# Kernel tuning notes

Measured on AMD Instinct MI355X. Metric: run time of the kernel, lower is better.

The kernel has to match this reference:

```python
import math
import jax, jax.numpy as jnp
import numpy as np

NEG_BIG = -1e12  # matches torch's -1000000000000.0 padding


def setup_inputs() -> dict:
    key = jax.random.key(0)
    k1, k2, k3 = jax.random.split(key, 3)
    bs, n_tok, n_heads, width = 1, 4096, 8, 64
    dst_mxlen, src_mxlen = 32, 64
    q = jax.random.normal(k1, (bs, n_tok, n_heads, width), dtype=jnp.float32)
    k = jax.random.normal(k2, (bs, n_tok, n_heads, width), dtype=jnp.float32)
    v = jax.random.normal(k3, (bs, n_tok, n_heads, width), dtype=jnp.float32)
    # Sliding-window COO: each dst attends to its dst_mxlen preceding tokens (clipped).
    dst = jnp.repeat(jnp.arange(n_tok, dtype=jnp.int32), dst_mxlen)
    cnt = jnp.tile(jnp.arange(dst_mxlen, dtype=jnp.int32), n_tok)
    src = jnp.clip(dst - cnt, 0, n_tok - 1)
    coo = jnp.stack([dst, src, cnt], axis=1)  # [cl, 3]
    return {"v": v, "q": q, "k": k, "coo": coo,
            "dst_mxlen": dst_mxlen, "src_mxlen": src_mxlen, "use_softmax": 1}


def reference(v, q, k, coo, dst_mxlen, src_mxlen, use_softmax):
    bs, n_tok, n_heads, width = q.shape
    cl = coo.shape[0]
    # [b, h, t, w] layout
    qq = jnp.transpose(q, (0, 2, 1, 3))[:, :, coo[:, 0], :]  # [b,h,cl,w]
    kk = jnp.transpose(k, (0, 2, 1, 3))[:, :, coo[:, 1], :]
    vv = jnp.transpose(v, (0, 2, 1, 3))
    scale = -1.0 / math.sqrt(width)
    ww = jnp.sum(jnp.abs(qq - kk), axis=-1) * scale  # [b,h,cl]
    # Padded softmax buffer, last slot is the (optional) softmax denominator pad.
    attn = jnp.full((bs, n_heads, n_tok, dst_mxlen + 1), NEG_BIG, dtype=q.dtype)
    attn = attn.at[:, :, coo[:, 0], coo[:, 2]].set(ww)
    if use_softmax:
        attn = attn.at[:, :, :, -1].set(0.0)
        attn_sm = jax.nn.softmax(attn, axis=-1)
    else:
        attn_sm = jnp.exp(attn)
    attn_sm = attn_sm[:, :, :, :-1]  # [b,h,t,s]
    # Scatter V into the padded buffer: vw[b,h,dst,cnt,:] = vv[b,h,src,:]
    vw = jnp.zeros((bs, n_heads, n_tok, dst_mxlen, width), dtype=q.dtype)
    vw = vw.at[:, :, coo[:, 0], coo[:, 2], :].set(vv[:, :, coo[:, 1], :])
    vo = jnp.einsum('bhds,bhdsw->bdhw', attn_sm, vw)
    return vo
```

## Files before the change

### kernel.cpp

```cpp
#include <hip/hip_runtime.h>
#include <math.h>


constexpr int H = 8;
constexpr int W = 64;
constexpr int TPW = 2;

template <int CTRL>
__device__ __forceinline__ float dpp_add(float x) {
    int xi = __builtin_bit_cast(int, x);
    int yi = __builtin_amdgcn_update_dpp(0, xi, CTRL, 0xf, 0xf, true);
    return x + __builtin_bit_cast(float, yi);
}

__device__ __forceinline__ float reduce16(float a) {
    a = dpp_add<0xB1>(a);
    a = dpp_add<0x4E>(a);
    a = dpp_add<0x141>(a);
    a = dpp_add<0x140>(a);
    return a;
}

__global__ __launch_bounds__(256) void l1attn_sparse_kernel(
    const float* __restrict__ v,
    const float* __restrict__ q,
    const float* __restrict__ k,
    const int*   __restrict__ p_dst_mxlen,
    const int*   __restrict__ p_use_softmax,
    float*       __restrict__ out,
    int n_tok)
{
    const int dst_mxlen = *p_dst_mxlen;
    const int use_sm    = *p_use_softmax;

    int bid = blockIdx.x;
    if ((gridDim.x & 7) == 0) {
        const int chunk = gridDim.x >> 3;
        bid = (bid & 7) * chunk + (bid >> 3);
    }

    const int wid  = bid * (blockDim.x >> 6) + (threadIdx.x >> 6);
    const int lane = threadIdx.x & 63;

    const int pairIdx = wid >> 1;
    const int t0 = pairIdx * TPW;
    if (t0 >= n_tok) return;
    const int h     = (wid & 1) * 4 + (lane >> 4);
    const int dbase = (lane & 15) * 4;

    float4 qv[TPW];
    #pragma unroll
    for (int j = 0; j < TPW; ++j) {
        int t = t0 + j; t = t < n_tok ? t : n_tok - 1;
        qv[j] = *reinterpret_cast<const float4*>(q + (t * H + h) * W + dbase);
    }

    float4 acc[TPW];
    float  sump[TPW];
    #pragma unroll
    for (int j = 0; j < TPW; ++j) { acc[j] = {0.f,0.f,0.f,0.f}; sump[j] = 0.f; }

    int s_lo = t0 - (dst_mxlen - 1); s_lo = s_lo < 0 ? 0 : s_lo;
    const int s_hi = (t0 + TPW - 1) < (n_tok - 1) ? (t0 + TPW - 1) : (n_tok - 1);

    #pragma unroll 4
    for (int s = s_lo; s <= s_hi; ++s) {
        const int base = (s * H + h) * W + dbase;
        const float4 kv = *reinterpret_cast<const float4*>(k + base);
        const float4 vv = *reinterpret_cast<const float4*>(v + base);

        #pragma unroll
        for (int j = 0; j < TPW; ++j) {
            const int t = t0 + j;
            float a = fabsf(qv[j].x - kv.x) + fabsf(qv[j].y - kv.y) +
                      fabsf(qv[j].z - kv.z) + fabsf(qv[j].w - kv.w);
            a = reduce16(a);

            float m;
            if (s == 0) {
                int mm = dst_mxlen - t;
                m = (float)(mm > 0 ? mm : 0);
            } else {
                const int c = t - s;
                m = (c >= 0 && c < dst_mxlen) ? 1.f : 0.f;
            }

            const float p = m * __expf(a * -0.125f);
            sump[j] += p;
            acc[j].x += p * vv.x; acc[j].y += p * vv.y;
            acc[j].z += p * vv.z; acc[j].w += p * vv.w;
        }
    }

    #pragma unroll
    for (int j = 0; j < TPW; ++j) {
        const int t = t0 + j;
        if (t < n_tok) {
            const float scale = use_sm ? 1.0f / (1.0f + sump[j]) : 1.0f;
            float4 o = {acc[j].x * scale, acc[j].y * scale,
                        acc[j].z * scale, acc[j].w * scale};
            *reinterpret_cast<float4*>(out + (t * H + h) * W + dbase) = o;
        }
    }
}

extern "C" void kernel_launch(void* const* d_in, const int* in_sizes, int n_in,
                              void* d_out, int out_size, void* d_ws, size_t ws_size,
                              hipStream_t stream) {
    const float* v   = (const float*)d_in[0];
    const float* q   = (const float*)d_in[1];
    const float* k   = (const float*)d_in[2];
    const int*   p_dst_mxlen = (const int*)d_in[4];
    const int*   p_use_sm    = (const int*)d_in[6];
    float* out = (float*)d_out;

    const int n_tok = in_sizes[1] / (H * W);

    const int pairs  = (n_tok + TPW - 1) / TPW;
    const int waves  = pairs * 2;
    const int blocks = (waves + 3) / 4;
    l1attn_sparse_kernel<<<blocks, 256, 0, stream>>>(
        v, q, k, p_dst_mxlen, p_use_sm, out, n_tok);
}
```

Baseline: 21.99 us.

## Split sliding window across two waves per head-half and combine partials via LDS

Each block now handles one token pair. Its four waves cover two head halves times two halves of the source window. The second window-half wave writes its partial accumulators and sums to shared memory, and after a barrier the first wave adds them and writes the output. This shortens each wave's serial loop and doubles the grid size to hide latency better, at the cost of a block barrier, LDS traffic, and half the waves idling during the epilogue.

```diff
diff --git a/kernel.cpp b/kernel.cpp
--- a/kernel.cpp
+++ b/kernel.cpp
@@ -39,13 +39,15 @@
         bid = (bid & 7) * chunk + (bid >> 3);
     }
 
-    const int wid  = bid * (blockDim.x >> 6) + (threadIdx.x >> 6);
+    const int sub  = threadIdx.x >> 6;
     const int lane = threadIdx.x & 63;
+    const int headhalf = sub >> 1;
+    const int winhalf  = sub & 1;
 
-    const int pairIdx = wid >> 1;
-    const int t0 = pairIdx * TPW;
+    const int t0 = bid * TPW;
     if (t0 >= n_tok) return;
-    const int h     = (wid & 1) * 4 + (lane >> 4);
+
+    const int h     = headhalf * 4 + (lane >> 4);
     const int dbase = (lane & 15) * 4;
 
     float4 qv[TPW];
@@ -62,9 +64,13 @@
 
     int s_lo = t0 - (dst_mxlen - 1); s_lo = s_lo < 0 ? 0 : s_lo;
     const int s_hi = (t0 + TPW - 1) < (n_tok - 1) ? (t0 + TPW - 1) : (n_tok - 1);
+    const int len  = s_hi - s_lo + 1;
+    const int half = (len + 1) >> 1;
+    const int my_lo = winhalf ? s_lo + half : s_lo;
+    const int my_hi = winhalf ? s_hi       : s_lo + half - 1;
 
     #pragma unroll 4
-    for (int s = s_lo; s <= s_hi; ++s) {
+    for (int s = my_lo; s <= my_hi; ++s) {
         const int base = (s * H + h) * W + dbase;
         const float4 kv = *reinterpret_cast<const float4*>(k + base);
         const float4 vv = *reinterpret_cast<const float4*>(v + base);
@@ -92,14 +98,34 @@
         }
     }
 
-    #pragma unroll
-    for (int j = 0; j < TPW; ++j) {
-        const int t = t0 + j;
-        if (t < n_tok) {
-            const float scale = use_sm ? 1.0f / (1.0f + sump[j]) : 1.0f;
-            float4 o = {acc[j].x * scale, acc[j].y * scale,
-                        acc[j].z * scale, acc[j].w * scale};
-            *reinterpret_cast<float4*>(out + (t * H + h) * W + dbase) = o;
+    __shared__ float lds[2][TPW][5][64];
+    if (winhalf == 1) {
+        #pragma unroll
+        for (int j = 0; j < TPW; ++j) {
+            lds[headhalf][j][0][lane] = acc[j].x;
+            lds[headhalf][j][1][lane] = acc[j].y;
+            lds[headhalf][j][2][lane] = acc[j].z;
+            lds[headhalf][j][3][lane] = acc[j].w;
+            lds[headhalf][j][4][lane] = sump[j];
+        }
+    }
+    __syncthreads();
+    if (winhalf == 0) {
+        #pragma unroll
+        for (int j = 0; j < TPW; ++j) {
+            acc[j].x += lds[headhalf][j][0][lane];
+            acc[j].y += lds[headhalf][j][1][lane];
+            acc[j].z += lds[headhalf][j][2][lane];
+            acc[j].w += lds[headhalf][j][3][lane];
+            sump[j]  += lds[headhalf][j][4][lane];
+
+            const int t = t0 + j;
+            if (t < n_tok) {
+                const float scale = use_sm ? 1.0f / (1.0f + sump[j]) : 1.0f;
+                float4 o = {acc[j].x * scale, acc[j].y * scale,
+                            acc[j].z * scale, acc[j].w * scale};
+                *reinterpret_cast<float4*>(out + (t * H + h) * W + dbase) = o;
+            }
         }
     }
 }
@@ -116,9 +142,7 @@
 
     const int n_tok = in_sizes[1] / (H * W);
 
-    const int pairs  = (n_tok + TPW - 1) / TPW;
-    const int waves  = pairs * 2;
-    const int blocks = (waves + 3) / 4;
+    const int blocks = (n_tok + TPW - 1) / TPW;
     l1attn_sparse_kernel<<<blocks, 256, 0, stream>>>(
         v, q, k, p_dst_mxlen, p_use_sm, out, n_tok);
 }
```

After: 20.51 us. 6.7% less time.

## Split window over four waves per token block with LDS reduction, packed math

Applied to the files above, without the earlier changes.

Each 512-thread block now handles four tokens across all heads. The source window is split into four quarters, one per wave, and the partial accumulators and softmax sums are combined through shared memory after a barrier. Sharing K/V across four tokens is meant to cut redundant loads, and the split is meant to shorten each wave's serial loop. The abs-diff and accumulate steps use packed 2-wide float vectors to target packed FP32 instructions. This adds LDS traffic, a block-wide sync, and idle waves during the final reduction.

```diff
diff --git a/kernel.cpp b/kernel.cpp
--- a/kernel.cpp
+++ b/kernel.cpp
@@ -2,9 +2,11 @@
 #include <math.h>
 
 
-constexpr int H = 8;
-constexpr int W = 64;
-constexpr int TPW = 2;
+typedef float v2f __attribute__((ext_vector_type(2)));
+
+constexpr int H   = 8;
+constexpr int W   = 64;
+constexpr int TPB = 4;
 
 template <int CTRL>
 __device__ __forceinline__ float dpp_add(float x) {
@@ -21,7 +23,17 @@
     return a;
 }
 
-__global__ __launch_bounds__(256) void l1attn_sparse_kernel(
+__device__ __forceinline__ float absdiff4(float4 qv, float4 kv) {
+    v2f q01 = {qv.x, qv.y}, q23 = {qv.z, qv.w};
+    v2f k01 = {kv.x, kv.y}, k23 = {kv.z, kv.w};
+    v2f d0 = q01 - k01, d1 = q23 - k23;
+    v2f a0 = __builtin_elementwise_max(d0, -d0);
+    v2f a1 = __builtin_elementwise_max(d1, -d1);
+    v2f ss = a0 + a1;
+    return ss.x + ss.y;
+}
+
+__global__ __launch_bounds__(512) void l1attn_sparse_kernel(
     const float* __restrict__ v,
     const float* __restrict__ q,
     const float* __restrict__ k,
@@ -39,67 +51,95 @@
         bid = (bid & 7) * chunk + (bid >> 3);
     }
 
-    const int wid  = bid * (blockDim.x >> 6) + (threadIdx.x >> 6);
+    const int sub  = threadIdx.x >> 6;
     const int lane = threadIdx.x & 63;
+    const int hh   = sub >> 2;
+    const int wq   = sub & 3;
 
-    const int pairIdx = wid >> 1;
-    const int t0 = pairIdx * TPW;
+    const int t0 = bid * TPB;
     if (t0 >= n_tok) return;
-    const int h     = (wid & 1) * 4 + (lane >> 4);
+
+    const int h     = hh * 4 + (lane >> 4);
     const int dbase = (lane & 15) * 4;
 
-    float4 qv[TPW];
+    float4 qv[TPB];
     #pragma unroll
-    for (int j = 0; j < TPW; ++j) {
+    for (int j = 0; j < TPB; ++j) {
         int t = t0 + j; t = t < n_tok ? t : n_tok - 1;
         qv[j] = *reinterpret_cast<const float4*>(q + (t * H + h) * W + dbase);
     }
 
-    float4 acc[TPW];
-    float  sump[TPW];
+    v2f   acc01[TPB], acc23[TPB];
+    float sump[TPB];
     #pragma unroll
-    for (int j = 0; j < TPW; ++j) { acc[j] = {0.f,0.f,0.f,0.f}; sump[j] = 0.f; }
+    for (int j = 0; j < TPB; ++j) {
+        acc01[j] = (v2f){0.f, 0.f}; acc23[j] = (v2f){0.f, 0.f}; sump[j] = 0.f;
+    }
 
     int s_lo = t0 - (dst_mxlen - 1); s_lo = s_lo < 0 ? 0 : s_lo;
-    const int s_hi = (t0 + TPW - 1) < (n_tok - 1) ? (t0 + TPW - 1) : (n_tok - 1);
+    int s_hi = t0 + TPB - 1; s_hi = s_hi < n_tok - 1 ? s_hi : n_tok - 1;
+    const int len  = s_hi - s_lo + 1;
+    const int qlen = (len + 3) >> 2;
+    const int my_lo = s_lo + wq * qlen;
+    int my_hi = my_lo + qlen - 1; my_hi = my_hi < s_hi ? my_hi : s_hi;
 
-    #pragma unroll 4
-    for (int s = s_lo; s <= s_hi; ++s) {
+    #pragma unroll 2
+    for (int s = my_lo; s <= my_hi; ++s) {
         const int base = (s * H + h) * W + dbase;
         const float4 kv = *reinterpret_cast<const float4*>(k + base);
         const float4 vv = *reinterpret_cast<const float4*>(v + base);
+        v2f v01 = {vv.x, vv.y}, v23 = {vv.z, vv.w};
 
         #pragma unroll
-        for (int j = 0; j < TPW; ++j) {
+        for (int j = 0; j < TPB; ++j) {
             const int t = t0 + j;
-            float a = fabsf(qv[j].x - kv.x) + fabsf(qv[j].y - kv.y) +
-                      fabsf(qv[j].z - kv.z) + fabsf(qv[j].w - kv.w);
-            a = reduce16(a);
+            float a = reduce16(absdiff4(qv[j], kv));
 
             float m;
             if (s == 0) {
                 int mm = dst_mxlen - t;
                 m = (float)(mm > 0 ? mm : 0);
             } else {
-                const int c = t - s;
-                m = (c >= 0 && c < dst_mxlen) ? 1.f : 0.f;
+                m = ((unsigned)(t - s) < (unsigned)dst_mxlen) ? 1.f : 0.f;
             }
 
             const float p = m * __expf(a * -0.125f);
             sump[j] += p;
-            acc[j].x += p * vv.x; acc[j].y += p * vv.y;
-            acc[j].z += p * vv.z; acc[j].w += p * vv.w;
+            acc01[j] += p * v01;
+            acc23[j] += p * v23;
         }
     }
 
-    #pragma unroll
-    for (int j = 0; j < TPW; ++j) {
-        const int t = t0 + j;
-        if (t < n_tok) {
-            const float scale = use_sm ? 1.0f / (1.0f + sump[j]) : 1.0f;
-            float4 o = {acc[j].x * scale, acc[j].y * scale,
-                        acc[j].z * scale, acc[j].w * scale};
-            *reinterpret_cast<float4*>(out + (t * H + h) * W + dbase) = o;
+    __shared__ float lds[3][2][TPB][5][64];
+    if (wq != 0) {
+        #pragma unroll
+        for (int j = 0; j < TPB; ++j) {
+            lds[wq - 1][hh][j][0][lane] = acc01[j].x;
+            lds[wq - 1][hh][j][1][lane] = acc01[j].y;
+            lds[wq - 1][hh][j][2][lane] = acc23[j].x;
+            lds[wq - 1][hh][j][3][lane] = acc23[j].y;
+            lds[wq - 1][hh][j][4][lane] = sump[j];
+        }
+    }
+    __syncthreads();
+    if (wq == 0) {
+        #pragma unroll
+        for (int j = 0; j < TPB; ++j) {
+            #pragma unroll
+            for (int qq = 0; qq < 3; ++qq) {
+                acc01[j].x += lds[qq][hh][j][0][lane];
+                acc01[j].y += lds[qq][hh][j][1][lane];
+                acc23[j].x += lds[qq][hh][j][2][lane];
+                acc23[j].y += lds[qq][hh][j][3][lane];
+                sump[j]    += lds[qq][hh][j][4][lane];
+            }
+            const int t = t0 + j;
+            if (t < n_tok) {
+                const float scale = use_sm ? 1.0f / (1.0f + sump[j]) : 1.0f;
+                float4 o = {acc01[j].x * scale, acc01[j].y * scale,
+                            acc23[j].x * scale, acc23[j].y * scale};
+                *reinterpret_cast<float4*>(out + (t * H + h) * W + dbase) = o;
+            }
         }
     }
 }
@@ -116,9 +156,7 @@
 
     const int n_tok = in_sizes[1] / (H * W);
 
-    const int pairs  = (n_tok + TPW - 1) / TPW;
-    const int waves  = pairs * 2;
-    const int blocks = (waves + 3) / 4;
-    l1attn_sparse_kernel<<<blocks, 256, 0, stream>>>(
+    const int blocks = (n_tok + TPB - 1) / TPB;
+    l1attn_sparse_kernel<<<blocks, 512, 0, stream>>>(
         v, q, k, p_dst_mxlen, p_use_sm, out, n_tok);
 }
```

Result: faster. 20.85 us (-5.2%).

## Switch to one token per wave with 1024-thread blocks and barrier-synced window loop

Applied to the files above, without the earlier changes.

Restructures the kernel so each wave handles a single destination token (8 tokens per 1024-thread block) and iterates directly over window offsets with clamped source indices, dropping the per-element mask logic. It uses packed two-wide float math for the L1 distance and accumulation, and exp2 with a prescaled constant. It inserts a workgroup barrier every four offsets so waves in a block stay in lockstep and share K/V cache lines. Cross-token K/V reuse within a wave is lost (each wave loads 32 rows per token rather than 33 per two tokens), and the barriers add synchronisation cost. Clamping to row 0 replicates the padded-position weighting implicitly.

```diff
diff --git a/kernel.cpp b/kernel.cpp
--- a/kernel.cpp
+++ b/kernel.cpp
@@ -2,9 +2,11 @@
 #include <math.h>
 
 
-constexpr int H = 8;
-constexpr int W = 64;
-constexpr int TPW = 2;
+typedef float v2f __attribute__((ext_vector_type(2)));
+
+constexpr int H   = 8;
+constexpr int W   = 64;
+constexpr int TPB = 8;
 
 template <int CTRL>
 __device__ __forceinline__ float dpp_add(float x) {
@@ -21,7 +23,17 @@
     return a;
 }
 
-__global__ __launch_bounds__(256) void l1attn_sparse_kernel(
+__device__ __forceinline__ float absdiff4(float4 qv, float4 kv) {
+    v2f q01 = {qv.x, qv.y}, q23 = {qv.z, qv.w};
+    v2f k01 = {kv.x, kv.y}, k23 = {kv.z, kv.w};
+    v2f d0 = q01 - k01, d1 = q23 - k23;
+    v2f a0 = __builtin_elementwise_max(d0, -d0);
+    v2f a1 = __builtin_elementwise_max(d1, -d1);
+    v2f ss = a0 + a1;
+    return ss.x + ss.y;
+}
+
+__global__ __launch_bounds__(1024) void l1attn_sparse_kernel(
     const float* __restrict__ v,
     const float* __restrict__ q,
     const float* __restrict__ k,
@@ -39,68 +51,59 @@
         bid = (bid & 7) * chunk + (bid >> 3);
     }
 
-    const int wid  = bid * (blockDim.x >> 6) + (threadIdx.x >> 6);
+    const int sub  = threadIdx.x >> 6;
     const int lane = threadIdx.x & 63;
+    const int hh   = sub & 1;
+    const int tloc = sub >> 1;
 
-    const int pairIdx = wid >> 1;
-    const int t0 = pairIdx * TPW;
-    if (t0 >= n_tok) return;
-    const int h     = (wid & 1) * 4 + (lane >> 4);
+    const int t     = bid * TPB + tloc;
+    const int valid = t < n_tok;
+    const int tc    = valid ? t : n_tok - 1;
+
+    const int h     = hh * 4 + (lane >> 4);
     const int dbase = (lane & 15) * 4;
+    const int hoff  = h * W + dbase;
 
-    float4 qv[TPW];
-    #pragma unroll
-    for (int j = 0; j < TPW; ++j) {
-        int t = t0 + j; t = t < n_tok ? t : n_tok - 1;
-        qv[j] = *reinterpret_cast<const float4*>(q + (t * H + h) * W + dbase);
+    const float4 qv =
+        *reinterpret_cast<const float4*>(q + tc * (H * W) + hoff);
+
+    v2f   acc01 = {0.f, 0.f}, acc23 = {0.f, 0.f};
+    float sump  = 0.f;
+
+    const int cmax = dst_mxlen;
+    for (int c0 = 0; c0 < cmax; c0 += 4) {
+        #pragma unroll
+        for (int bpair = 0; bpair < 2; ++bpair) {
+            const int ca = c0 + bpair * 2;
+            int s0 = tc - ca;     s0 = s0 > 0 ? s0 : 0;
+            int s1 = tc - ca - 1; s1 = s1 > 0 ? s1 : 0;
+            const int b0 = s0 * (H * W) + hoff;
+            const int b1 = s1 * (H * W) + hoff;
+            const float4 k0 = *reinterpret_cast<const float4*>(k + b0);
+            const float4 v0 = *reinterpret_cast<const float4*>(v + b0);
+            const float4 k1 = *reinterpret_cast<const float4*>(k + b1);
+            const float4 v1 = *reinterpret_cast<const float4*>(v + b1);
+
+            float a0 = reduce16(absdiff4(qv, k0));
+            float p0 = exp2f(a0 * -0.18033688f);
+            sump += p0;
+            v2f v001 = {v0.x, v0.y}, v023 = {v0.z, v0.w};
+            acc01 += p0 * v001; acc23 += p0 * v023;
+
+            float a1 = reduce16(absdiff4(qv, k1));
+            float p1 = exp2f(a1 * -0.18033688f);
+            sump += p1;
+            v2f v101 = {v1.x, v1.y}, v123 = {v1.z, v1.w};
+            acc01 += p1 * v101; acc23 += p1 * v123;
+        }
+        __builtin_amdgcn_s_barrier();
     }
 
-    float4 acc[TPW];
-    float  sump[TPW];
-    #pragma unroll
-    for (int j = 0; j < TPW; ++j) { acc[j] = {0.f,0.f,0.f,0.f}; sump[j] = 0.f; }
-
-    int s_lo = t0 - (dst_mxlen - 1); s_lo = s_lo < 0 ? 0 : s_lo;
-    const int s_hi = (t0 + TPW - 1) < (n_tok - 1) ? (t0 + TPW - 1) : (n_tok - 1);
-
-    #pragma unroll 4
-    for (int s = s_lo; s <= s_hi; ++s) {
-        const int base = (s * H + h) * W + dbase;
-        const float4 kv = *reinterpret_cast<const float4*>(k + base);
-        const float4 vv = *reinterpret_cast<const float4*>(v + base);
-
-        #pragma unroll
-        for (int j = 0; j < TPW; ++j) {
-            const int t = t0 + j;
-            float a = fabsf(qv[j].x - kv.x) + fabsf(qv[j].y - kv.y) +
-                      fabsf(qv[j].z - kv.z) + fabsf(qv[j].w - kv.w);
-            a = reduce16(a);
-
-            float m;
-            if (s == 0) {
-                int mm = dst_mxlen - t;
-                m = (float)(mm > 0 ? mm : 0);
-            } else {
-                const int c = t - s;
-                m = (c >= 0 && c < dst_mxlen) ? 1.f : 0.f;
-            }
-
-            const float p = m * __expf(a * -0.125f);
-            sump[j] += p;
-            acc[j].x += p * vv.x; acc[j].y += p * vv.y;
-            acc[j].z += p * vv.z; acc[j].w += p * vv.w;
-        }
-    }
-
-    #pragma unroll
-    for (int j = 0; j < TPW; ++j) {
-        const int t = t0 + j;
-        if (t < n_tok) {
-            const float scale = use_sm ? 1.0f / (1.0f + sump[j]) : 1.0f;
-            float4 o = {acc[j].x * scale, acc[j].y * scale,
-                        acc[j].z * scale, acc[j].w * scale};
-            *reinterpret_cast<float4*>(out + (t * H + h) * W + dbase) = o;
-        }
+    if (valid) {
+        const float scale = use_sm ? 1.0f / (1.0f + sump) : 1.0f;
+        float4 o = {acc01.x * scale, acc01.y * scale,
+                    acc23.x * scale, acc23.y * scale};
+        *reinterpret_cast<float4*>(out + t * (H * W) + hoff) = o;
     }
 }
 
@@ -116,9 +119,7 @@
 
     const int n_tok = in_sizes[1] / (H * W);
 
-    const int pairs  = (n_tok + TPW - 1) / TPW;
-    const int waves  = pairs * 2;
-    const int blocks = (waves + 3) / 4;
-    l1attn_sparse_kernel<<<blocks, 256, 0, stream>>>(
+    const int blocks = (n_tok + TPB - 1) / TPB;
+    l1attn_sparse_kernel<<<blocks, 1024, 0, stream>>>(
         v, q, k, p_dst_mxlen, p_use_sm, out, n_tok);
 }
```

Measured after the change: 24.27 us. 1.1x slower.
